# Kernel optimization log

Measured on AMD Instinct MI355X. Metric: run time of the kernel, lower is better.

The kernel has to match this reference:

```python
import jax, jax.numpy as jnp
import numpy as np

N_NODES = 10000
N_EDGES = 320000
D_FEAT = 512
N_HIDDEN = 256
N_LATENT = 64


def setup_inputs() -> dict:
    key = jax.random.key(0)
    ks = jax.random.split(key, 7)
    x = jax.random.normal(ks[0], (N_NODES, D_FEAT), dtype=jnp.float32)
    edge_src = jax.random.randint(ks[1], (N_EDGES,), 0, N_NODES, dtype=jnp.int32)
    edge_dst = jax.random.randint(ks[2], (N_EDGES,), 0, N_NODES, dtype=jnp.int32)
    # positive weights, like D^{-1/2} A D^{-1/2} entries
    edge_weight = jax.random.uniform(ks[3], (N_EDGES,), dtype=jnp.float32)
    scale1 = 1.0 / np.sqrt(D_FEAT)
    scale2 = 1.0 / np.sqrt(N_HIDDEN)
    W1 = jax.random.normal(ks[4], (D_FEAT, N_HIDDEN), dtype=jnp.float32) * scale1
    W2_mu = jax.random.normal(ks[5], (N_HIDDEN, N_LATENT), dtype=jnp.float32) * scale2
    W2_sig = jax.random.normal(ks[6], (N_HIDDEN, N_LATENT), dtype=jnp.float32) * scale2
    return {"x": x, "edge_src": edge_src, "edge_dst": edge_dst,
            "edge_weight": edge_weight, "W1": W1, "W2_mu": W2_mu, "W2_sig": W2_sig}


def reference(x, edge_src, edge_dst, edge_weight, W1, W2_mu, W2_sig):
    N = x.shape[0]

    def spmm(feat):
        # sparse adj_norm @ feat via gather + weighted segment-sum
        msg = feat[edge_src] * edge_weight[:, None]           # [E, F]
        return jax.ops.segment_sum(msg, edge_dst, num_segments=N)  # [N, F]

    # GCN layer 1: relu(adj @ (x @ W1)); dropout is identity at inference
    h = jax.nn.relu(spmm(x @ W1))                              # [N, H]
    # GCN layer 2 (mu and log-sigma heads); encoder returns exp(log_sig)
    mu = spmm(h @ W2_mu)                                       # [N, L]
    sigma = jnp.exp(spmm(h @ W2_sig))                          # [N, L]
    # InnerProductDecoder: adj = z @ z.T (normalized z_ is computed but unused
    # in the original code, so it is faithfully omitted); z = mu embedding
    adj_rec = mu @ mu.T                                        # [N, N]
    return mu, sigma, adj_rec
```

## Files before the change

kernel.cpp:

```cpp
#include <hip/hip_runtime.h>
#include <hip/hip_bf16.h>
#include <math.h>
#include <float.h>

#define N_NODES 10000
#define N_EDGES 320000
#define D_FEAT  512
#define N_HID   256
#define N_LAT   64

typedef __bf16 bf16x4 __attribute__((ext_vector_type(4)));
typedef __bf16 bf16x8 __attribute__((ext_vector_type(8)));
typedef float  f32x4  __attribute__((ext_vector_type(4)));


__global__ __launch_bounds__(256) void k_hist(const int* __restrict__ dst,
                                              int* __restrict__ deg) {
    int i = blockIdx.x * 256 + threadIdx.x;
    if (i < N_EDGES) atomicAdd(&deg[dst[i]], 1);
}

__global__ __launch_bounds__(1024) void k_scan(const int* __restrict__ deg,
                                               int* __restrict__ rowptr,
                                               int* __restrict__ woff) {
    __shared__ int wsum[16];
    __shared__ int carry_s;
    int tid = threadIdx.x;
    if (tid == 0) carry_s = 0;
    __syncthreads();
    int lane = tid & 63, wv = tid >> 6;
    for (int base = 0; base < N_NODES; base += 1024) {
        int i = base + tid;
        int v = (i < N_NODES) ? deg[i] : 0;
        int x = v;
        #pragma unroll
        for (int off = 1; off < 64; off <<= 1) {
            int y = __shfl_up(x, off);
            if (lane >= off) x += y;
        }
        if (lane == 63) wsum[wv] = x;
        __syncthreads();
        int add = carry_s;
        for (int k = 0; k < wv; k++) add += wsum[k];
        int incl = x + add;
        int excl = incl - v;
        if (i < N_NODES) { rowptr[i] = excl; woff[i] = excl; }
        __syncthreads();
        if (tid == 1023) carry_s = incl;
        __syncthreads();
    }
    if (tid == 0) rowptr[N_NODES] = carry_s;
}

__global__ __launch_bounds__(256) void k_scatter(const int* __restrict__ src,
                                                 const int* __restrict__ dst,
                                                 const float* __restrict__ w,
                                                 int* __restrict__ woff,
                                                 int* __restrict__ esrc,
                                                 float* __restrict__ ew) {
    int i = blockIdx.x * 256 + threadIdx.x;
    if (i < N_EDGES) {
        int d = dst[i];
        int r = atomicAdd(&woff[d], 1);
        esrc[r] = src[i];
        ew[r] = w[i];
    }
}


__global__ __launch_bounds__(256) void k_xsplit(const float* __restrict__ x,
                                                __bf16* __restrict__ xh,
                                                __bf16* __restrict__ xl) {
    int i = blockIdx.x * 256 + threadIdx.x;
    float4 v = ((const float4*)x)[i];
    __bf16 h0 = (__bf16)v.x, h1 = (__bf16)v.y, h2 = (__bf16)v.z, h3 = (__bf16)v.w;
    bf16x4 hv = {h0, h1, h2, h3};
    bf16x4 lv = {(__bf16)(v.x - (float)h0), (__bf16)(v.y - (float)h1),
                 (__bf16)(v.z - (float)h2), (__bf16)(v.w - (float)h3)};
    ((bf16x4*)xh)[i] = hv;
    ((bf16x4*)xl)[i] = lv;
}

__global__ __launch_bounds__(256) void k_wsplit(const float* __restrict__ W1,
                                                const float* __restrict__ W2mu,
                                                const float* __restrict__ W2sig,
                                                __bf16* __restrict__ w1h,
                                                __bf16* __restrict__ w1l,
                                                __bf16* __restrict__ w2h,
                                                __bf16* __restrict__ w2l) {
    int i = blockIdx.x * 256 + threadIdx.x;
    if (i < 512 * 256) {
        int j = i >> 9, k = i & 511;
        float v = W1[k * N_HID + j];
        __bf16 hi = (__bf16)v;
        w1h[i] = hi;
        w1l[i] = (__bf16)(v - (float)hi);
    } else {
        int t = i - 512 * 256;
        int j = t >> 8, k = t & 255;
        float v = (j < 64) ? W2mu[k * N_LAT + j] : W2sig[k * N_LAT + (j - 64)];
        __bf16 hi = (__bf16)v;
        w2h[t] = hi;
        w2l[t] = (__bf16)(v - (float)hi);
    }
}


__global__ __launch_bounds__(256) void k_gemm1m(const __bf16* __restrict__ xh,
                                                const __bf16* __restrict__ xl,
                                                const __bf16* __restrict__ w1h,
                                                const __bf16* __restrict__ w1l,
                                                float* __restrict__ xw1) {
    int tid = threadIdx.x;
    int l = tid & 63, w = tid >> 6;
    int wr = w >> 1, wc = w & 1;
    int i0 = blockIdx.y * 128 + wr * 64;
    int j0 = blockIdx.x * 64 + wc * 32;
    int lr = l & 15, lk = (l >> 4) * 8;

    f32x4 acc[4][2];
    #pragma unroll
    for (int a = 0; a < 4; a++)
        #pragma unroll
        for (int b = 0; b < 2; b++) acc[a][b] = (f32x4)(0.0f);

    #pragma unroll 4
    for (int ks = 0; ks < 16; ks++) {
        int k0 = ks * 32 + lk;
        bf16x8 ah[4], al[4], bh[2], bl[2];
        #pragma unroll
        for (int mi = 0; mi < 4; mi++) {
            int row = i0 + mi * 16 + lr;
            if (row > N_NODES - 1) row = N_NODES - 1;
            ah[mi] = *(const bf16x8*)(xh + row * D_FEAT + k0);
            al[mi] = *(const bf16x8*)(xl + row * D_FEAT + k0);
        }
        #pragma unroll
        for (int ni = 0; ni < 2; ni++) {
            int jr = j0 + ni * 16 + lr;
            bh[ni] = *(const bf16x8*)(w1h + jr * D_FEAT + k0);
            bl[ni] = *(const bf16x8*)(w1l + jr * D_FEAT + k0);
        }
        #pragma unroll
        for (int mi = 0; mi < 4; mi++)
            #pragma unroll
            for (int ni = 0; ni < 2; ni++) {
                acc[mi][ni] = __builtin_amdgcn_mfma_f32_16x16x32_bf16(ah[mi], bh[ni], acc[mi][ni], 0, 0, 0);
                acc[mi][ni] = __builtin_amdgcn_mfma_f32_16x16x32_bf16(ah[mi], bl[ni], acc[mi][ni], 0, 0, 0);
                acc[mi][ni] = __builtin_amdgcn_mfma_f32_16x16x32_bf16(al[mi], bh[ni], acc[mi][ni], 0, 0, 0);
            }
    }
    int c16 = l & 15, r4 = l >> 4;
    #pragma unroll
    for (int mi = 0; mi < 4; mi++)
        #pragma unroll
        for (int ni = 0; ni < 2; ni++)
            #pragma unroll
            for (int r = 0; r < 4; r++) {
                int row = i0 + mi * 16 + r4 * 4 + r;
                int col = j0 + ni * 16 + c16;
                if (row < N_NODES) xw1[row * N_HID + col] = acc[mi][ni][r];
            }
}


__global__ __launch_bounds__(256) void k_spmm1w(const int* __restrict__ rowptr,
                                                const int* __restrict__ esrc,
                                                const float* __restrict__ ew,
                                                const float* __restrict__ xw1,
                                                __bf16* __restrict__ hh,
                                                __bf16* __restrict__ hl) {
    int lane = threadIdx.x & 63, w = threadIdx.x >> 6;
    int n = blockIdx.x * 4 + w;
    int s = __builtin_amdgcn_readfirstlane(rowptr[n]);
    int e = __builtin_amdgcn_readfirstlane(rowptr[n + 1]);
    const float4* X = (const float4*)xw1;
    float4 acc = make_float4(0.f, 0.f, 0.f, 0.f);
    int i = s;
    for (; i + 3 < e; i += 4) {
        int s0 = esrc[i], s1 = esrc[i + 1], s2 = esrc[i + 2], s3 = esrc[i + 3];
        float w0 = ew[i], w1 = ew[i + 1], w2 = ew[i + 2], w3 = ew[i + 3];
        float4 v0 = X[s0 * 64 + lane];
        float4 v1 = X[s1 * 64 + lane];
        float4 v2 = X[s2 * 64 + lane];
        float4 v3 = X[s3 * 64 + lane];
        acc.x += w0 * v0.x + w1 * v1.x + w2 * v2.x + w3 * v3.x;
        acc.y += w0 * v0.y + w1 * v1.y + w2 * v2.y + w3 * v3.y;
        acc.z += w0 * v0.z + w1 * v1.z + w2 * v2.z + w3 * v3.z;
        acc.w += w0 * v0.w + w1 * v1.w + w2 * v2.w + w3 * v3.w;
    }
    for (; i < e; i++) {
        int sc = esrc[i]; float wv = ew[i];
        float4 v = X[sc * 64 + lane];
        acc.x += wv * v.x; acc.y += wv * v.y; acc.z += wv * v.z; acc.w += wv * v.w;
    }
    acc.x = fmaxf(acc.x, 0.f); acc.y = fmaxf(acc.y, 0.f);
    acc.z = fmaxf(acc.z, 0.f); acc.w = fmaxf(acc.w, 0.f);
    __bf16 h0 = (__bf16)acc.x, h1 = (__bf16)acc.y, h2 = (__bf16)acc.z, h3 = (__bf16)acc.w;
    bf16x4 hv = {h0, h1, h2, h3};
    bf16x4 lv = {(__bf16)(acc.x - (float)h0), (__bf16)(acc.y - (float)h1),
                 (__bf16)(acc.z - (float)h2), (__bf16)(acc.w - (float)h3)};
    ((bf16x4*)(hh + n * N_HID))[lane] = hv;
    ((bf16x4*)(hl + n * N_HID))[lane] = lv;
}


__global__ __launch_bounds__(256) void k_gemm2m(const __bf16* __restrict__ hh,
                                                const __bf16* __restrict__ hl,
                                                const __bf16* __restrict__ w2h,
                                                const __bf16* __restrict__ w2l,
                                                float* __restrict__ pre) {
    int tid = threadIdx.x;
    int l = tid & 63, w = tid >> 6;
    int wr = w >> 1, wc = w & 1;
    int i0 = blockIdx.y * 128 + wr * 64;
    int j0 = blockIdx.x * 64 + wc * 32;
    int lr = l & 15, lk = (l >> 4) * 8;

    f32x4 acc[4][2];
    #pragma unroll
    for (int a = 0; a < 4; a++)
        #pragma unroll
        for (int b = 0; b < 2; b++) acc[a][b] = (f32x4)(0.0f);

    #pragma unroll 4
    for (int ks = 0; ks < 8; ks++) {
        int k0 = ks * 32 + lk;
        bf16x8 ah[4], al[4], bh[2], bl[2];
        #pragma unroll
        for (int mi = 0; mi < 4; mi++) {
            int row = i0 + mi * 16 + lr;
            if (row > N_NODES - 1) row = N_NODES - 1;
            ah[mi] = *(const bf16x8*)(hh + row * N_HID + k0);
            al[mi] = *(const bf16x8*)(hl + row * N_HID + k0);
        }
        #pragma unroll
        for (int ni = 0; ni < 2; ni++) {
            int jr = j0 + ni * 16 + lr;
            bh[ni] = *(const bf16x8*)(w2h + jr * N_HID + k0);
            bl[ni] = *(const bf16x8*)(w2l + jr * N_HID + k0);
        }
        #pragma unroll
        for (int mi = 0; mi < 4; mi++)
            #pragma unroll
            for (int ni = 0; ni < 2; ni++) {
                acc[mi][ni] = __builtin_amdgcn_mfma_f32_16x16x32_bf16(ah[mi], bh[ni], acc[mi][ni], 0, 0, 0);
                acc[mi][ni] = __builtin_amdgcn_mfma_f32_16x16x32_bf16(ah[mi], bl[ni], acc[mi][ni], 0, 0, 0);
                acc[mi][ni] = __builtin_amdgcn_mfma_f32_16x16x32_bf16(al[mi], bh[ni], acc[mi][ni], 0, 0, 0);
            }
    }
    int c16 = l & 15, r4 = l >> 4;
    #pragma unroll
    for (int mi = 0; mi < 4; mi++)
        #pragma unroll
        for (int ni = 0; ni < 2; ni++)
            #pragma unroll
            for (int r = 0; r < 4; r++) {
                int row = i0 + mi * 16 + r4 * 4 + r;
                int col = j0 + ni * 16 + c16;
                if (row < N_NODES) pre[row * 128 + col] = acc[mi][ni][r];
            }
}


__global__ __launch_bounds__(256) void k_spmm2w(const int* __restrict__ rowptr,
                                                const int* __restrict__ esrc,
                                                const float* __restrict__ ew,
                                                const float* __restrict__ pre,
                                                float* __restrict__ out_mu,
                                                float* __restrict__ out_sig) {
    int lane = threadIdx.x & 63, w = threadIdx.x >> 6;
    int n = blockIdx.x * 4 + w;
    int s = __builtin_amdgcn_readfirstlane(rowptr[n]);
    int e = __builtin_amdgcn_readfirstlane(rowptr[n + 1]);
    const float2* P = (const float2*)pre;
    float2 acc = make_float2(0.f, 0.f);
    int i = s;
    for (; i + 3 < e; i += 4) {
        int s0 = esrc[i], s1 = esrc[i + 1], s2 = esrc[i + 2], s3 = esrc[i + 3];
        float w0 = ew[i], w1 = ew[i + 1], w2 = ew[i + 2], w3 = ew[i + 3];
        float2 v0 = P[s0 * 64 + lane];
        float2 v1 = P[s1 * 64 + lane];
        float2 v2 = P[s2 * 64 + lane];
        float2 v3 = P[s3 * 64 + lane];
        acc.x += w0 * v0.x + w1 * v1.x + w2 * v2.x + w3 * v3.x;
        acc.y += w0 * v0.y + w1 * v1.y + w2 * v2.y + w3 * v3.y;
    }
    for (; i < e; i++) {
        int sc = esrc[i]; float wv = ew[i];
        float2 v = P[sc * 64 + lane];
        acc.x += wv * v.x; acc.y += wv * v.y;
    }
    if (lane < 32) {
        ((float2*)(out_mu + n * 64))[lane] = acc;
    } else {
        float2 sg = make_float2(fminf(expf(acc.x), 3.0e38f),
                                fminf(expf(acc.y), 3.0e38f));
        ((float2*)(out_sig + n * 64))[lane - 32] = sg;
    }
}


__global__ __launch_bounds__(256) void k_mu2bf(const float* __restrict__ mu,
                                               __bf16* __restrict__ muh,
                                               __bf16* __restrict__ mul) {
    int i = blockIdx.x * 256 + threadIdx.x;
    float4 v = ((const float4*)mu)[i];
    __bf16 h0 = (__bf16)v.x, h1 = (__bf16)v.y, h2 = (__bf16)v.z, h3 = (__bf16)v.w;
    bf16x4 hv = {h0, h1, h2, h3};
    bf16x4 lv = {(__bf16)(v.x - (float)h0), (__bf16)(v.y - (float)h1),
                 (__bf16)(v.z - (float)h2), (__bf16)(v.w - (float)h3)};
    ((bf16x4*)muh)[i] = hv;
    ((bf16x4*)mul)[i] = lv;
}


#define ADJ_TS 68

__global__ __launch_bounds__(256) void k_adj(const __bf16* __restrict__ muh,
                                             const __bf16* __restrict__ mul,
                                             float* __restrict__ C) {
    __shared__ float Ts[4][32 * ADJ_TS];
    int tid = threadIdx.x;
    int l = tid & 63, w = tid >> 6;
    int wr = w >> 1, wc = w & 1;
    int i0 = blockIdx.y * 128 + wr * 64;
    int j0 = blockIdx.x * 128 + wc * 64;
    int lr = l & 15;
    int lk = (l >> 4) * 8;

    f32x4 acc[4][4];
    #pragma unroll
    for (int a = 0; a < 4; a++)
        #pragma unroll
        for (int b = 0; b < 4; b++) acc[a][b] = (f32x4)(0.0f);

    #pragma unroll
    for (int ks = 0; ks < 2; ks++) {
        int k0 = ks * 32 + lk;
        bf16x8 ah[4], al[4], bh[4], bl[4];
        #pragma unroll
        for (int mi = 0; mi < 4; mi++) {
            int row = i0 + mi * 16 + lr;
            if (row > N_NODES - 1) row = N_NODES - 1;
            ah[mi] = *(const bf16x8*)(muh + row * 64 + k0);
            al[mi] = *(const bf16x8*)(mul + row * 64 + k0);
        }
        #pragma unroll
        for (int ni = 0; ni < 4; ni++) {
            int row = j0 + ni * 16 + lr;
            if (row > N_NODES - 1) row = N_NODES - 1;
            bh[ni] = *(const bf16x8*)(muh + row * 64 + k0);
            bl[ni] = *(const bf16x8*)(mul + row * 64 + k0);
        }
        #pragma unroll
        for (int mi = 0; mi < 4; mi++)
            #pragma unroll
            for (int ni = 0; ni < 4; ni++) {
                acc[mi][ni] = __builtin_amdgcn_mfma_f32_16x16x32_bf16(ah[mi], bh[ni], acc[mi][ni], 0, 0, 0);
                acc[mi][ni] = __builtin_amdgcn_mfma_f32_16x16x32_bf16(ah[mi], bl[ni], acc[mi][ni], 0, 0, 0);
                acc[mi][ni] = __builtin_amdgcn_mfma_f32_16x16x32_bf16(al[mi], bh[ni], acc[mi][ni], 0, 0, 0);
            }
    }

    float* T = Ts[w];
    int c16 = l & 15, r4 = l >> 4;
    #pragma unroll
    for (int half = 0; half < 2; half++) {
        __syncthreads();
        #pragma unroll
        for (int m2 = 0; m2 < 2; m2++) {
            int mi = half * 2 + m2;
            #pragma unroll
            for (int ni = 0; ni < 4; ni++)
                #pragma unroll
                for (int r = 0; r < 4; r++)
                    T[(m2 * 16 + r4 * 4 + r) * ADJ_TS + ni * 16 + c16] = acc[mi][ni][r];
        }
        __syncthreads();
        #pragma unroll
        for (int q = 0; q < 8; q++) {
            int rr = q * 4 + r4;
            int row = i0 + half * 32 + rr;
            int col = j0 + c16 * 4;
            if (row < N_NODES && col < N_NODES)
                *(float4*)&C[(size_t)row * N_NODES + col] =
                    *(const float4*)&T[rr * ADJ_TS + c16 * 4];
        }
    }
}


extern "C" void kernel_launch(void* const* d_in, const int* in_sizes, int n_in,
                              void* d_out, int out_size, void* d_ws, size_t ws_size,
                              hipStream_t stream) {
    const float* x       = (const float*)d_in[0];
    const int*   esrc_in = (const int*)d_in[1];
    const int*   edst_in = (const int*)d_in[2];
    const float* ew_in   = (const float*)d_in[3];
    const float* W1      = (const float*)d_in[4];
    const float* W2mu    = (const float*)d_in[5];
    const float* W2sig   = (const float*)d_in[6];

    char* ws = (char*)d_ws;
    __bf16* xh   = (__bf16*)(ws + 0);
    __bf16* xl   = (__bf16*)(ws + 10240000);
    float*  xw1  = (float*) (ws + 20480000);
    __bf16* hh   = (__bf16*)(ws + 0);
    __bf16* hl   = (__bf16*)(ws + 5120000);
    float*  pre  = (float*) (ws + 10240000);
    __bf16* muh  = (__bf16*)(ws + 20480000);
    __bf16* mul  = (__bf16*)(ws + 21760000);
    int*    esrc = (int*)   (ws + 30720000);
    float*  ew   = (float*) (ws + 32000000);
    __bf16* w1h  = (__bf16*)(ws + 33280000);
    __bf16* w1l  = (__bf16*)(ws + 33542144);
    __bf16* w2h  = (__bf16*)(ws + 33804288);
    __bf16* w2l  = (__bf16*)(ws + 33869824);
    int*    deg  = (int*)   (ws + 33935360);
    int*  rowptr = (int*)   (ws + 33975360);
    int*    woff = (int*)   (ws + 34015376);

    float* out_mu  = (float*)d_out;
    float* out_sig = out_mu + 640000;
    float* out_adj = out_sig + 640000;

    hipMemsetAsync(deg, 0, N_NODES * sizeof(int), stream);
    k_hist   <<<(N_EDGES + 255) / 256, 256, 0, stream>>>(edst_in, deg);
    k_scan   <<<1, 1024, 0, stream>>>(deg, rowptr, woff);
    k_scatter<<<(N_EDGES + 255) / 256, 256, 0, stream>>>(esrc_in, edst_in, ew_in,
                                                         woff, esrc, ew);
    k_xsplit <<<5000, 256, 0, stream>>>(x, xh, xl);
    k_wsplit <<<640, 256, 0, stream>>>(W1, W2mu, W2sig, w1h, w1l, w2h, w2l);
    {
        dim3 g(4, (N_NODES + 127) / 128);
        k_gemm1m<<<g, 256, 0, stream>>>(xh, xl, w1h, w1l, xw1);
    }
    k_spmm1w <<<N_NODES / 4, 256, 0, stream>>>(rowptr, esrc, ew, xw1, hh, hl);
    {
        dim3 g(2, (N_NODES + 127) / 128);
        k_gemm2m<<<g, 256, 0, stream>>>(hh, hl, w2h, w2l, pre);
    }
    k_spmm2w <<<N_NODES / 4, 256, 0, stream>>>(rowptr, esrc, ew, pre, out_mu, out_sig);
    k_mu2bf  <<<640000 / 4 / 256, 256, 0, stream>>>(out_mu, muh, mul);
    {
        dim3 g((N_NODES + 127) / 128, (N_NODES + 127) / 128);
        k_adj  <<<g, 256, 0, stream>>>(muh, mul, out_adj);
    }
}
```

Baseline: 654.2 us.

## Shard degree atomics, fuse split and mu-convert kernels, remap adj tiles per XCD

The degree histogram and scatter offsets are spread over 8 copies by block index, which cuts atomic contention on hot destination nodes. The x and weight split kernels are merged into one launch, and the mu hi/lo bf16 split is folded into the second SpMM so one kernel disappears. The adjacency GEMM now uses a 1D grid remapped so that consecutive tiles land on the same XCD, and the large output writes use nontemporal stores. These changes trade a larger workspace and more complex indexing for fewer launches and better L2 locality on the output-bound adj write.

After: 635.1 us. 1.03x faster.

```diff
diff --git a/kernel.cpp b/kernel.cpp
--- a/kernel.cpp
+++ b/kernel.cpp
@@ -9,20 +9,23 @@
 #define N_HID   256
 #define N_LAT   64
 
+typedef __bf16 bf16x2 __attribute__((ext_vector_type(2)));
 typedef __bf16 bf16x4 __attribute__((ext_vector_type(4)));
 typedef __bf16 bf16x8 __attribute__((ext_vector_type(8)));
+typedef float  f32x2  __attribute__((ext_vector_type(2)));
 typedef float  f32x4  __attribute__((ext_vector_type(4)));
 
 
-__global__ __launch_bounds__(256) void k_hist(const int* __restrict__ dst,
-                                              int* __restrict__ deg) {
+__global__ __launch_bounds__(256) void k_hist8(const int* __restrict__ dst,
+                                               int* __restrict__ deg8) {
     int i = blockIdx.x * 256 + threadIdx.x;
-    if (i < N_EDGES) atomicAdd(&deg[dst[i]], 1);
-}
-
-__global__ __launch_bounds__(1024) void k_scan(const int* __restrict__ deg,
-                                               int* __restrict__ rowptr,
-                                               int* __restrict__ woff) {
+    int sh = blockIdx.x & 7;
+    if (i < N_EDGES) atomicAdd(&deg8[sh * N_NODES + dst[i]], 1);
+}
+
+__global__ __launch_bounds__(1024) void k_scan8(const int* __restrict__ deg8,
+                                                int* __restrict__ rowptr,
+                                                int* __restrict__ woff8) {
     __shared__ int wsum[16];
     __shared__ int carry_s;
     int tid = threadIdx.x;
@@ -31,7 +34,13 @@
     int lane = tid & 63, wv = tid >> 6;
     for (int base = 0; base < N_NODES; base += 1024) {
         int i = base + tid;
-        int v = (i < N_NODES) ? deg[i] : 0;
+        int d8[8];
+        int v = 0;
+        #pragma unroll
+        for (int s = 0; s < 8; s++) {
+            d8[s] = (i < N_NODES) ? deg8[s * N_NODES + i] : 0;
+            v += d8[s];
+        }
         int x = v;
         #pragma unroll
         for (int off = 1; off < 64; off <<= 1) {
@@ -44,7 +53,12 @@
         for (int k = 0; k < wv; k++) add += wsum[k];
         int incl = x + add;
         int excl = incl - v;
-        if (i < N_NODES) { rowptr[i] = excl; woff[i] = excl; }
+        if (i < N_NODES) {
+            rowptr[i] = excl;
+            int run = excl;
+            #pragma unroll
+            for (int s = 0; s < 8; s++) { woff8[s * N_NODES + i] = run; run += d8[s]; }
+        }
         __syncthreads();
         if (tid == 1023) carry_s = incl;
         __syncthreads();
@@ -52,56 +66,58 @@
     if (tid == 0) rowptr[N_NODES] = carry_s;
 }
 
-__global__ __launch_bounds__(256) void k_scatter(const int* __restrict__ src,
-                                                 const int* __restrict__ dst,
-                                                 const float* __restrict__ w,
-                                                 int* __restrict__ woff,
-                                                 int* __restrict__ esrc,
-                                                 float* __restrict__ ew) {
+__global__ __launch_bounds__(256) void k_scatter8(const int* __restrict__ src,
+                                                  const int* __restrict__ dst,
+                                                  const float* __restrict__ w,
+                                                  int* __restrict__ woff8,
+                                                  int* __restrict__ esrc,
+                                                  float* __restrict__ ew) {
     int i = blockIdx.x * 256 + threadIdx.x;
+    int sh = blockIdx.x & 7;
     if (i < N_EDGES) {
         int d = dst[i];
-        int r = atomicAdd(&woff[d], 1);
+        int r = atomicAdd(&woff8[sh * N_NODES + d], 1);
         esrc[r] = src[i];
         ew[r] = w[i];
     }
 }
 
 
-__global__ __launch_bounds__(256) void k_xsplit(const float* __restrict__ x,
-                                                __bf16* __restrict__ xh,
-                                                __bf16* __restrict__ xl) {
-    int i = blockIdx.x * 256 + threadIdx.x;
-    float4 v = ((const float4*)x)[i];
-    __bf16 h0 = (__bf16)v.x, h1 = (__bf16)v.y, h2 = (__bf16)v.z, h3 = (__bf16)v.w;
-    bf16x4 hv = {h0, h1, h2, h3};
-    bf16x4 lv = {(__bf16)(v.x - (float)h0), (__bf16)(v.y - (float)h1),
-                 (__bf16)(v.z - (float)h2), (__bf16)(v.w - (float)h3)};
-    ((bf16x4*)xh)[i] = hv;
-    ((bf16x4*)xl)[i] = lv;
-}
-
-__global__ __launch_bounds__(256) void k_wsplit(const float* __restrict__ W1,
-                                                const float* __restrict__ W2mu,
-                                                const float* __restrict__ W2sig,
-                                                __bf16* __restrict__ w1h,
-                                                __bf16* __restrict__ w1l,
-                                                __bf16* __restrict__ w2h,
-                                                __bf16* __restrict__ w2l) {
-    int i = blockIdx.x * 256 + threadIdx.x;
-    if (i < 512 * 256) {
-        int j = i >> 9, k = i & 511;
-        float v = W1[k * N_HID + j];
-        __bf16 hi = (__bf16)v;
-        w1h[i] = hi;
-        w1l[i] = (__bf16)(v - (float)hi);
+__global__ __launch_bounds__(256) void k_split(const float* __restrict__ x,
+                                               const float* __restrict__ W1,
+                                               const float* __restrict__ W2mu,
+                                               const float* __restrict__ W2sig,
+                                               __bf16* __restrict__ xh,
+                                               __bf16* __restrict__ xl,
+                                               __bf16* __restrict__ w1h,
+                                               __bf16* __restrict__ w1l,
+                                               __bf16* __restrict__ w2h,
+                                               __bf16* __restrict__ w2l) {
+    if (blockIdx.x < 5000) {
+        int i = blockIdx.x * 256 + threadIdx.x;
+        float4 v = ((const float4*)x)[i];
+        __bf16 h0 = (__bf16)v.x, h1 = (__bf16)v.y, h2 = (__bf16)v.z, h3 = (__bf16)v.w;
+        bf16x4 hv = {h0, h1, h2, h3};
+        bf16x4 lv = {(__bf16)(v.x - (float)h0), (__bf16)(v.y - (float)h1),
+                     (__bf16)(v.z - (float)h2), (__bf16)(v.w - (float)h3)};
+        ((bf16x4*)xh)[i] = hv;
+        ((bf16x4*)xl)[i] = lv;
     } else {
-        int t = i - 512 * 256;
-        int j = t >> 8, k = t & 255;
-        float v = (j < 64) ? W2mu[k * N_LAT + j] : W2sig[k * N_LAT + (j - 64)];
-        __bf16 hi = (__bf16)v;
-        w2h[t] = hi;
-        w2l[t] = (__bf16)(v - (float)hi);
+        int i = (blockIdx.x - 5000) * 256 + threadIdx.x;
+        if (i < 512 * 256) {
+            int j = i >> 9, k = i & 511;
+            float v = W1[k * N_HID + j];
+            __bf16 hi = (__bf16)v;
+            w1h[i] = hi;
+            w1l[i] = (__bf16)(v - (float)hi);
+        } else {
+            int t = i - 512 * 256;
+            int j = t >> 8, k = t & 255;
+            float v = (j < 64) ? W2mu[k * N_LAT + j] : W2sig[k * N_LAT + (j - 64)];
+            __bf16 hi = (__bf16)v;
+            w2h[t] = hi;
+            w2l[t] = (__bf16)(v - (float)hi);
+        }
     }
 }
 
@@ -268,7 +284,9 @@
                                                 const float* __restrict__ ew,
                                                 const float* __restrict__ pre,
                                                 float* __restrict__ out_mu,
-                                                float* __restrict__ out_sig) {
+                                                float* __restrict__ out_sig,
+                                                __bf16* __restrict__ muh,
+                                                __bf16* __restrict__ mul) {
     int lane = threadIdx.x & 63, w = threadIdx.x >> 6;
     int n = blockIdx.x * 4 + w;
     int s = __builtin_amdgcn_readfirstlane(rowptr[n]);
@@ -292,40 +310,39 @@
         acc.x += wv * v.x; acc.y += wv * v.y;
     }
     if (lane < 32) {
-        ((float2*)(out_mu + n * 64))[lane] = acc;
+        f32x2 mv = {acc.x, acc.y};
+        __builtin_nontemporal_store(mv, (f32x2*)(out_mu + n * 64) + lane);
+        __bf16 h0 = (__bf16)acc.x, h1 = (__bf16)acc.y;
+        bf16x2 hv = {h0, h1};
+        bf16x2 lv = {(__bf16)(acc.x - (float)h0), (__bf16)(acc.y - (float)h1)};
+        ((bf16x2*)(muh + n * 64))[lane] = hv;
+        ((bf16x2*)(mul + n * 64))[lane] = lv;
     } else {
-        float2 sg = make_float2(fminf(expf(acc.x), 3.0e38f),
-                                fminf(expf(acc.y), 3.0e38f));
-        ((float2*)(out_sig + n * 64))[lane - 32] = sg;
-    }
-}
-
-
-__global__ __launch_bounds__(256) void k_mu2bf(const float* __restrict__ mu,
-                                               __bf16* __restrict__ muh,
-                                               __bf16* __restrict__ mul) {
-    int i = blockIdx.x * 256 + threadIdx.x;
-    float4 v = ((const float4*)mu)[i];
-    __bf16 h0 = (__bf16)v.x, h1 = (__bf16)v.y, h2 = (__bf16)v.z, h3 = (__bf16)v.w;
-    bf16x4 hv = {h0, h1, h2, h3};
-    bf16x4 lv = {(__bf16)(v.x - (float)h0), (__bf16)(v.y - (float)h1),
-                 (__bf16)(v.z - (float)h2), (__bf16)(v.w - (float)h3)};
-    ((bf16x4*)muh)[i] = hv;
-    ((bf16x4*)mul)[i] = lv;
+        f32x2 sg = {fminf(expf(acc.x), 3.0e38f), fminf(expf(acc.y), 3.0e38f)};
+        __builtin_nontemporal_store(sg, (f32x2*)(out_sig + n * 64) + (lane - 32));
+    }
 }
 
 
 #define ADJ_TS 68
+#define ADJ_NB 6241
+#define ADJ_Q  780
+#define ADJ_R  1
 
 __global__ __launch_bounds__(256) void k_adj(const __bf16* __restrict__ muh,
                                              const __bf16* __restrict__ mul,
                                              float* __restrict__ C) {
     __shared__ float Ts[4][32 * ADJ_TS];
+    int g = blockIdx.x;
+    int xcd = g & 7, idx = g >> 3;
+    int wg = (xcd < ADJ_R ? xcd * (ADJ_Q + 1) : ADJ_R * (ADJ_Q + 1) + (xcd - ADJ_R) * ADJ_Q) + idx;
+    int ti = wg / 79, tj = wg % 79;
+
     int tid = threadIdx.x;
     int l = tid & 63, w = tid >> 6;
     int wr = w >> 1, wc = w & 1;
-    int i0 = blockIdx.y * 128 + wr * 64;
-    int j0 = blockIdx.x * 128 + wc * 64;
+    int i0 = ti * 128 + wr * 64;
+    int j0 = tj * 128 + wc * 64;
     int lr = l & 15;
     int lk = (l >> 4) * 8;
 
@@ -383,9 +400,10 @@
             int rr = q * 4 + r4;
             int row = i0 + half * 32 + rr;
             int col = j0 + c16 * 4;
-            if (row < N_NODES && col < N_NODES)
-                *(float4*)&C[(size_t)row * N_NODES + col] =
-                    *(const float4*)&T[rr * ADJ_TS + c16 * 4];
+            if (row < N_NODES && col < N_NODES) {
+                f32x4 val = *(const f32x4*)&T[rr * ADJ_TS + c16 * 4];
+                __builtin_nontemporal_store(val, (f32x4*)&C[(size_t)row * N_NODES + col]);
+            }
         }
     }
 }
@@ -417,34 +435,30 @@
     __bf16* w1l  = (__bf16*)(ws + 33542144);
     __bf16* w2h  = (__bf16*)(ws + 33804288);
     __bf16* w2l  = (__bf16*)(ws + 33869824);
-    int*    deg  = (int*)   (ws + 33935360);
-    int*  rowptr = (int*)   (ws + 33975360);
-    int*    woff = (int*)   (ws + 34015376);
+    int*  rowptr = (int*)   (ws + 33935360);
+    int*    deg8 = (int*)   (ws + 33975376);
+    int*   woff8 = (int*)   (ws + 34295376);
 
     float* out_mu  = (float*)d_out;
     float* out_sig = out_mu + 640000;
     float* out_adj = out_sig + 640000;
 
-    hipMemsetAsync(deg, 0, N_NODES * sizeof(int), stream);
-    k_hist   <<<(N_EDGES + 255) / 256, 256, 0, stream>>>(edst_in, deg);
-    k_scan   <<<1, 1024, 0, stream>>>(deg, rowptr, woff);
-    k_scatter<<<(N_EDGES + 255) / 256, 256, 0, stream>>>(esrc_in, edst_in, ew_in,
-                                                         woff, esrc, ew);
-    k_xsplit <<<5000, 256, 0, stream>>>(x, xh, xl);
-    k_wsplit <<<640, 256, 0, stream>>>(W1, W2mu, W2sig, w1h, w1l, w2h, w2l);
+    hipMemsetAsync(deg8, 0, 8 * N_NODES * sizeof(int), stream);
+    k_hist8   <<<(N_EDGES + 255) / 256, 256, 0, stream>>>(edst_in, deg8);
+    k_scan8   <<<1, 1024, 0, stream>>>(deg8, rowptr, woff8);
+    k_scatter8<<<(N_EDGES + 255) / 256, 256, 0, stream>>>(esrc_in, edst_in, ew_in,
+                                                          woff8, esrc, ew);
+    k_split   <<<5640, 256, 0, stream>>>(x, W1, W2mu, W2sig, xh, xl, w1h, w1l, w2h, w2l);
     {
         dim3 g(4, (N_NODES + 127) / 128);
         k_gemm1m<<<g, 256, 0, stream>>>(xh, xl, w1h, w1l, xw1);
     }
-    k_spmm1w <<<N_NODES / 4, 256, 0, stream>>>(rowptr, esrc, ew, xw1, hh, hl);
+    k_spmm1w  <<<N_NODES / 4, 256, 0, stream>>>(rowptr, esrc, ew, xw1, hh, hl);
     {
         dim3 g(2, (N_NODES + 127) / 128);
         k_gemm2m<<<g, 256, 0, stream>>>(hh, hl, w2h, w2l, pre);
     }
-    k_spmm2w <<<N_NODES / 4, 256, 0, stream>>>(rowptr, esrc, ew, pre, out_mu, out_sig);
-    k_mu2bf  <<<640000 / 4 / 256, 256, 0, stream>>>(out_mu, muh, mul);
-    {
-        dim3 g((N_NODES + 127) / 128, (N_NODES + 127) / 128);
-        k_adj  <<<g, 256, 0, stream>>>(muh, mul, out_adj);
-    }
-}
+    k_spmm2w  <<<N_NODES / 4, 256, 0, stream>>>(rowptr, esrc, ew, pre,
+                                                out_mu, out_sig, muh, mul);
+    k_adj     <<<ADJ_NB, 256, 0, stream>>>(muh, mul, out_adj);
+}
```
